# Optimization experiments

Hardware: AMD Instinct MI355X
Metric: run time of the kernel (lower is better)

## Reference

```python
import jax, jax.numpy as jnp
import numpy as np

HO, WO = 64, 64
SHARPNESS = 150.0


def _stereographic_grid(ho, wo):
    # Matches create_normal_grid(..., 'stereographic'); torch.meshgrid 'ij':
    # v varies over rows (ho), u over cols (wo).
    v, u = np.meshgrid(np.arange(ho), np.arange(wo), indexing='ij')
    p = 4.0 * ((u + 0.5) / wo - 0.5)
    q = -4.0 * ((v + 0.5) / ho - 0.5)
    d = 1.0 + p ** 2 + q ** 2
    z = -(-1.0 + p ** 2 + q ** 2) / d
    m = (z > 0.0).astype(np.float32)
    x = 2.0 * p / d * m
    y = 2.0 * q / d * m
    z = z * m
    return np.stack([x, y, z], axis=-1).reshape(-1, 3).astype(np.float32)  # [ho*wo,3]


_GRID = _stereographic_grid(HO, WO)
_IDX = np.nonzero(np.any(_GRID != 0, axis=-1))[0]  # static valid-query indices [N]
_QN = _GRID[_IDX]  # [N,3]


def setup_inputs() -> dict:
    key = jax.random.key(0)
    k1, k2, k3 = jax.random.split(key, 3)
    bs, c, h, w = 2, 64, 192, 192
    in_fea_map = jax.random.normal(k1, (bs, c, h, w), dtype=jnp.float32)
    nrm = jax.random.normal(k2, (bs, 3, h, w), dtype=jnp.float32)
    in_normal_map = nrm / (jnp.linalg.norm(nrm, axis=1, keepdims=True) + 1e-8)
    in_mask_map = (jax.random.uniform(k3, (bs, 1, h, w)) > 0.2).astype(jnp.float32)
    log_query_norm = jnp.full((1,), np.log(SHARPNESS), dtype=jnp.float32)
    return {"in_fea_map": in_fea_map, "in_normal_map": in_normal_map,
            "in_mask_map": in_mask_map, "log_query_norm": log_query_norm}


def reference(in_fea_map, in_normal_map, in_mask_map, log_query_norm):
    bs, c, h, w = in_fea_map.shape
    hw = h * w
    qn = jnp.asarray(_QN, dtype=in_fea_map.dtype)  # [N,3] static valid queries
    vals = in_fea_map.reshape(bs, c, hw).transpose(0, 2, 1)       # [bs,HW,c]
    key_n = in_normal_map.reshape(bs, 3, hw)                       # [bs,3,HW]
    cos = jnp.einsum('nd,bdm->bnm', qn, key_n)                     # [bs,N,HW]
    dps = cos / np.float32(np.sqrt(3.0))
    dps = dps - jnp.max(dps, axis=-1, keepdims=True)
    w_ = jnp.exp(jnp.exp(log_query_norm) * dps)                    # dropout in eval = identity
    w_ = w_ * in_mask_map.reshape(bs, 1, hw)
    weights = w_ / (jnp.sum(w_, axis=-1, keepdims=True) + 1e-9)    # [bs,N,HW]
    mapped = weights @ vals                                        # [bs,N,c]
    mapped = jnp.concatenate([jnp.broadcast_to(qn, (bs,) + qn.shape), mapped], axis=-1)
    # variance map over last 3 feature channels
    mean = mapped[..., -3:]
    sq_mean = weights @ (vals[..., -3:] ** 2)
    var = jnp.sum(sq_mean - mean ** 2, axis=-1, keepdims=True)
    mapped = jnp.concatenate([var, mapped], axis=-1)
    # cosine map
    rm_cos = jnp.sum(weights * cos, axis=-1, keepdims=True)
    mapped = jnp.concatenate([rm_cos, mapped], axis=-1)            # [bs,N,c+5]
    C = mapped.shape[-1]
    out = jnp.zeros((bs, HO * WO, C), mapped.dtype).at[:, _IDX, :].set(mapped)
    return out.transpose(0, 2, 1).reshape(bs, C, HO, WO)
```

## Files before the change

kernel.cpp:

```cpp
#include <hip/hip_runtime.h>
#include <hip/hip_bf16.h>
#include <cstdint>
#include <cstddef>

#define HW 36864
#define QT 64
#define NCHA 69
#define NCHK 576

constexpr bool is_valid_px(int v, int u) {
  int a = 2 * u - 63, b = 2 * v - 63;
  return a * a + b * b < 1024;
}
constexpr int count_valid() {
  int n = 0;
  for (int v = 0; v < 64; ++v)
    for (int u = 0; u < 64; ++u)
      if (is_valid_px(v, u)) ++n;
  return n;
}
constexpr int NV  = count_valid();
constexpr int NQT = (NV + QT - 1) / QT;
constexpr int NQP = NQT * QT;
constexpr int PLANE = 2 * NQP * NCHA;

constexpr size_t BM_SHORTS  = (size_t)2 * NCHK * 80 * 64;
constexpr size_t BM_BYTES   = BM_SHORTS * 2;
constexpr size_t NV_BYTES   = (size_t)2 * HW * 4 * 4;
constexpr size_t PART_OFF   = BM_BYTES + NV_BYTES;

struct QTab {
  short idx[NQP];
  short rank[4096];
};
constexpr QTab make_qtab() {
  QTab t{};
  int n = 0;
  for (int p = 0; p < 4096; ++p) {
    int v = p >> 6, u = p & 63;
    if (is_valid_px(v, u)) { t.idx[n] = (short)p; t.rank[p] = (short)n; ++n; }
    else t.rank[p] = -1;
  }
  for (int i = n; i < NQP; ++i) t.idx[i] = -1;
  return t;
}
__constant__ QTab g_qtab = make_qtab();

typedef short short8 __attribute__((ext_vector_type(8)));
typedef float f32x4  __attribute__((ext_vector_type(4)));

__device__ __forceinline__ unsigned short f2b(float f) {
  unsigned int u = __float_as_uint(f);
  u += 0x7FFFu + ((u >> 16) & 1u);
  return (unsigned short)(u >> 16);
}
__device__ __forceinline__ ushort2 f2b2(float a, float b) {
  __hip_bfloat162 h = __float22bfloat162_rn(make_float2(a, b));
  return *(ushort2*)&h;
}
__device__ __forceinline__ void pix2qn(int pix, float& x, float& y, float& z) {
  x = 0.f; y = 0.f; z = 0.f;
  if (pix >= 0) {
    int v = pix >> 6, u = pix & 63;
    float p = (float)(2 * u - 63) * (1.0f / 32.0f);
    float q = -(float)(2 * v - 63) * (1.0f / 32.0f);
    float d = 1.0f + p * p + q * q;
    x = 2.0f * p / d; y = 2.0f * q / d; z = (1.0f - p * p - q * q) / d;
  }
}

#define PREP_BM_BLKS 2880
#define PREP_NV_BLKS 288

__global__ __launch_bounds__(256) void prep_kernel(
    const float* __restrict__ fea,
    const float* __restrict__ nrm,
    const float* __restrict__ msk,
    const float* __restrict__ lqn,
    unsigned short* __restrict__ Bm,
    float* __restrict__ nv)
{
  const float Cc = __expf(lqn[0]) * 0.57735026919f;
  if (blockIdx.x < PREP_BM_BLKS) {
    int gid = blockIdx.x * 256 + threadIdx.x;
    int g   = gid & 7;
    int row = (gid >> 3) % 80;
    int chk = ((gid >> 3) / 80) % NCHK;
    int b   = gid / (8 * 80 * NCHK);
    int px0 = chk * 64 + g * 8;
    float v[8];
    if (row < 64) {
      const float* p = fea + ((size_t)b * 64 + row) * HW + px0;
      #pragma unroll
      for (int i = 0; i < 8; ++i) v[i] = p[i];
    } else if (row < 67) {
      const float* p = fea + ((size_t)b * 64 + (61 + row - 64)) * HW + px0;
      #pragma unroll
      for (int i = 0; i < 8; ++i) { float x = p[i]; v[i] = x * x; }
    } else if (row < 70) {
      const float* p = nrm + ((size_t)b * 3 + (row - 67)) * HW + px0;
      #pragma unroll
      for (int i = 0; i < 8; ++i) v[i] = p[i];
    } else {
      float c = (row == 70) ? 1.0f : 0.0f;
      #pragma unroll
      for (int i = 0; i < 8; ++i) v[i] = c;
    }
    short8 o;
    #pragma unroll
    for (int p2 = 0; p2 < 4; ++p2) {
      ushort2 pr = f2b2(v[2 * p2], v[2 * p2 + 1]);
      o[2 * p2] = (short)pr.x; o[2 * p2 + 1] = (short)pr.y;
    }
    *(short8*)&Bm[(((size_t)b * NCHK + chk) * 80 + row) * 64 + g * 8] = o;
  } else {
    int p = (blockIdx.x - PREP_BM_BLKS) * 256 + threadIdx.x;
    int b = p / HW, px = p % HW;
    float nx = nrm[((size_t)b * 3 + 0) * HW + px];
    float ny = nrm[((size_t)b * 3 + 1) * HW + px];
    float nz = nrm[((size_t)b * 3 + 2) * HW + px];
    float mk = msk[(size_t)b * HW + px];
    float bias = -Cc + (mk > 0.5f ? 0.f : -2000.f);
    *(float4*)&nv[(size_t)p * 4] = make_float4(Cc * nx, Cc * ny, Cc * nz, bias);
  }
}

template<int KSC>
__global__ __launch_bounds__(256, 4) void partial_kernel(
    const unsigned short* __restrict__ Bm,
    const float* __restrict__ nv,
    float* __restrict__ part)
{
  constexpr int SLICE  = HW / KSC;
  constexpr int NCHUNK = SLICE / 64;

  __shared__ __align__(16) unsigned short v_s[2][80][72];

  const int bx  = blockIdx.x;
  const int cls = bx & 7;
  const int r0  = bx >> 3;
  const int qt  = r0 % NQT;
  const int sh  = r0 / NQT;
  const int s   = sh * 8 + cls;
  const int b   = s / KSC;
  const int ks  = s % KSC;

  const int t    = threadIdx.x;
  const int wv   = t >> 6;
  const int Mh   = wv & 1;
  const int kko  = (wv >> 1) * 32;
  const int l    = t & 63;
  const int lq   = l >> 4;
  const int mrow = l & 15;

  float qx[2], qy[2], qz[2];
  pix2qn(g_qtab.idx[qt * QT + 32 * Mh + mrow],      qx[0], qy[0], qz[0]);
  pix2qn(g_qtab.idx[qt * QT + 32 * Mh + 16 + mrow], qx[1], qy[1], qz[1]);

  const int g0r = t >> 3,          g0c = (t & 7) * 8;
  const int g1r = (t + 256) >> 3,  g1c = g0c;
  const int g2r = (t + 512) >> 3;

  f32x4 acc[2][5];
  #pragma unroll
  for (int h = 0; h < 2; ++h)
    #pragma unroll
    for (int nt = 0; nt < 5; ++nt) acc[h][nt] = (f32x4)(0.0f);

  short8 pB[3];

  const int ckb = ks * NCHUNK;
  const float4* nvb = (const float4*)nv
      + ((size_t)b * HW + (size_t)ckb * 64 + (size_t)(kko + 8 * lq));

  auto load_chunk = [&](int ck) {
    int chkAbs = ckb + ck;
    const unsigned short* src = Bm + ((size_t)b * NCHK + chkAbs) * (80 * 64);
    pB[0] = *(const short8*)(src + (size_t)(t)       * 8);
    pB[1] = *(const short8*)(src + (size_t)(t + 256) * 8);
    if (t < 128) pB[2] = *(const short8*)(src + (size_t)(t + 512) * 8);
  };
  auto store_chunk = [&](int buf) {
    *(short8*)&v_s[buf][g0r][g0c] = pB[0];
    *(short8*)&v_s[buf][g1r][g1c] = pB[1];
    if (t < 128) *(short8*)&v_s[buf][g2r][g0c] = pB[2];
  };

  load_chunk(0);
  store_chunk(0);
  __syncthreads();

  for (int ck = 0; ck < NCHUNK; ++ck) {
    const int buf = ck & 1;
    if (ck + 1 < NCHUNK) load_chunk(ck + 1);

    const float4* nvp = nvb + (size_t)ck * 64;
    float e0[8], e1[8];
    #pragma unroll
    for (int j = 0; j < 8; ++j) {
      const float4 nvv = nvp[j];
      float t0 = fmaf(qx[0], nvv.x, fmaf(qy[0], nvv.y, fmaf(qz[0], nvv.z, nvv.w)));
      float t1 = fmaf(qx[1], nvv.x, fmaf(qy[1], nvv.y, fmaf(qz[1], nvv.z, nvv.w)));
      e0[j] = __expf(t0);
      e1[j] = __expf(t1);
    }
    short8 a0, a1;
    #pragma unroll
    for (int p = 0; p < 4; ++p) {
      ushort2 p0 = f2b2(e0[2 * p], e0[2 * p + 1]);
      ushort2 p1 = f2b2(e1[2 * p], e1[2 * p + 1]);
      a0[2 * p] = (short)p0.x; a0[2 * p + 1] = (short)p0.y;
      a1[2 * p] = (short)p1.x; a1[2 * p + 1] = (short)p1.y;
    }
    #pragma unroll
    for (int nt = 0; nt < 5; ++nt) {
      short8 bb = *(const short8*)&v_s[buf][16 * nt + mrow][kko + 8 * lq];
      acc[0][nt] = __builtin_amdgcn_mfma_f32_16x16x32_bf16(a0, bb, acc[0][nt], 0, 0, 0);
      acc[1][nt] = __builtin_amdgcn_mfma_f32_16x16x32_bf16(a1, bb, acc[1][nt], 0, 0, 0);
    }

    if (ck + 1 < NCHUNK) {
      store_chunk(buf ^ 1);
      __syncthreads();
    }
  }

  __syncthreads();
  float* scr = (float*)&v_s[0][0][0];
  float* exs = scr + 64 * 80;

  if (kko) {
    #pragma unroll
    for (int h = 0; h < 2; ++h)
      #pragma unroll
      for (int nt = 0; nt < 5; ++nt)
        #pragma unroll
        for (int rr = 0; rr < 4; ++rr) {
          int qloc = 32 * Mh + 16 * h + 4 * lq + rr;
          scr[qloc * 80 + 16 * nt + mrow] = acc[h][nt][rr];
        }
  }
  __syncthreads();
  const size_t pbase = (size_t)ks * PLANE + ((size_t)b * NQP + (size_t)(qt * QT)) * NCHA;
  if (!kko) {
    #pragma unroll
    for (int h = 0; h < 2; ++h) {
      #pragma unroll
      for (int nt = 0; nt < 5; ++nt)
        #pragma unroll
        for (int rr = 0; rr < 4; ++rr) {
          int qloc = 32 * Mh + 16 * h + 4 * lq + rr;
          acc[h][nt][rr] += scr[qloc * 80 + 16 * nt + mrow];
        }
      #pragma unroll
      for (int nt = 0; nt < 4; ++nt)
        #pragma unroll
        for (int rr = 0; rr < 4; ++rr) {
          int qloc = 32 * Mh + 16 * h + 4 * lq + rr;
          part[pbase + (size_t)qloc * NCHA + (size_t)(16 * nt + mrow)] = acc[h][nt][rr];
        }
      if (mrow < 7) {
        #pragma unroll
        for (int rr = 0; rr < 4; ++rr)
          exs[(32 * Mh + 16 * h + 4 * lq + rr) * 9 + mrow] = acc[h][4][rr];
      }
    }
  }
  __syncthreads();
  if (t < 64) {
    float gx, gy, gz;
    pix2qn(g_qtab.idx[qt * QT + t], gx, gy, gz);
    const float* E = exs + t * 9;
    float swc = gx * E[3] + gy * E[4] + gz * E[5];
    size_t o = pbase + (size_t)t * NCHA;
    part[o + 64] = E[0];
    part[o + 65] = E[1];
    part[o + 66] = E[2];
    part[o + 67] = swc;
    part[o + 68] = E[6];
  }
}

#define NFIN (2 * NQT * 16)
#define NTAIL (2 * NFIN)

__global__ __launch_bounds__(256) void finalize_kernel(
    const float* __restrict__ part,
    float* __restrict__ out,
    int ksc)
{
  const int blk = blockIdx.x;
  const int t   = threadIdx.x;

  if (blk < NFIN) {
    __shared__ float sm[4][NCHA];
    const int b   = blk / (NQT * 16);
    const int rem = blk % (NQT * 16);
    const int qt  = rem >> 4;
    const int qr  = rem & 15;
    const int q0  = qt * QT + qr * 4;

    const size_t colbase = ((size_t)b * NQP + (size_t)q0) * NCHA;
    for (int i = t; i < 4 * NCHA; i += 256) {
      float sv = 0.f;
      const size_t off = colbase + (size_t)i;
      #pragma unroll 8
      for (int k = 0; k < ksc; ++k) sv += part[(size_t)k * PLANE + off];
      sm[0][i] = sv;
    }
    __syncthreads();

    for (int i = t; i < 4 * NCHA; i += 256) {
      const int ql = i / NCHA;
      const int oc = i % NCHA;
      const int pix = g_qtab.idx[q0 + ql];
      if (pix < 0) continue;
      const float* A = sm[ql];
      const float inv = 1.0f / (A[68] + 1e-9f);
      float gx, gy, gz;
      pix2qn(pix, gx, gy, gz);
      float val;
      if (oc == 0)      val = A[67] * inv;
      else if (oc == 1) {
        val = 0.f;
        #pragma unroll
        for (int j = 0; j < 3; ++j) {
          float m  = A[61 + j] * inv;
          float sq = A[64 + j] * inv;
          val += sq - m * m;
        }
      }
      else if (oc == 2) val = gx;
      else if (oc == 3) val = gy;
      else if (oc == 4) val = gz;
      else              val = A[oc - 5] * inv;
      out[((size_t)b * NCHA + (size_t)oc) * 4096 + pix] = val;
    }
  } else {
    const int start = (blk - NFIN) * 256 + t;
    const int strd  = (NTAIL - NFIN) * 256;
    const int TOT   = 2 * NCHA * 4096;
    for (int i = start; i < TOT; i += strd) {
      if (g_qtab.rank[i & 4095] < 0) out[i] = 0.0f;
    }
  }
}

extern "C" void kernel_launch(void* const* d_in, const int* in_sizes, int n_in,
                              void* d_out, int out_size, void* d_ws, size_t ws_size,
                              hipStream_t stream) {
  const float* fea = (const float*)d_in[0];
  const float* nrm = (const float*)d_in[1];
  const float* msk = (const float*)d_in[2];
  const float* lqn = (const float*)d_in[3];
  unsigned short* Bm = (unsigned short*)d_ws;
  float* nv   = (float*)((char*)d_ws + BM_BYTES);
  float* part = (float*)((char*)d_ws + PART_OFF);
  float* out  = (float*)d_out;

  prep_kernel<<<dim3(PREP_BM_BLKS + PREP_NV_BLKS), 256, 0, stream>>>(
      fea, nrm, msk, lqn, Bm, nv);

  const size_t need64 = PART_OFF + (size_t)PLANE * 64 * sizeof(float);
  const size_t need32 = PART_OFF + (size_t)PLANE * 32 * sizeof(float);
  if (ws_size >= need64) {
    partial_kernel<64><<<dim3(2 * 64 * NQT), 256, 0, stream>>>(Bm, nv, part);
    finalize_kernel<<<dim3(NTAIL), 256, 0, stream>>>(part, out, 64);
  } else if (ws_size >= need32) {
    partial_kernel<32><<<dim3(2 * 32 * NQT), 256, 0, stream>>>(Bm, nv, part);
    finalize_kernel<<<dim3(NTAIL), 256, 0, stream>>>(part, out, 32);
  } else {
    partial_kernel<16><<<dim3(2 * 16 * NQT), 256, 0, stream>>>(Bm, nv, part);
    finalize_kernel<<<dim3(NTAIL), 256, 0, stream>>>(part, out, 16);
  }
}
```

Measured before the change: 118.7 us.

## Fuse bf16 prep into partial kernel and widen query tile to 128

Removes the separate prep kernel and its workspace round trip. The partial kernel now loads fp32 features, normals and mask directly, converts them to bf16 and builds the scaled-normal table in shared memory. The query tile doubles to 128, so each wave owns 32 queries over the full 64-pixel chunk, and the cross-wave K reduction through shared memory goes away. The cost is repeated fp32 loads and conversions per query tile (fewer tiles now) and larger global loads per block, in exchange for one less launch and no intermediate buffer.

Result: faster. 107.9 us (-9.1%).

```diff
diff --git a/kernel.cpp b/kernel.cpp
--- a/kernel.cpp
+++ b/kernel.cpp
@@ -4,9 +4,8 @@
 #include <cstddef>
 
 #define HW 36864
-#define QT 64
+#define QT 128
 #define NCHA 69
-#define NCHK 576
 
 constexpr bool is_valid_px(int v, int u) {
   int a = 2 * u - 63, b = 2 * v - 63;
@@ -23,11 +22,6 @@
 constexpr int NQT = (NV + QT - 1) / QT;
 constexpr int NQP = NQT * QT;
 constexpr int PLANE = 2 * NQP * NCHA;
-
-constexpr size_t BM_SHORTS  = (size_t)2 * NCHK * 80 * 64;
-constexpr size_t BM_BYTES   = BM_SHORTS * 2;
-constexpr size_t NV_BYTES   = (size_t)2 * HW * 4 * 4;
-constexpr size_t PART_OFF   = BM_BYTES + NV_BYTES;
 
 struct QTab {
   short idx[NQP];
@@ -49,14 +43,17 @@
 typedef short short8 __attribute__((ext_vector_type(8)));
 typedef float f32x4  __attribute__((ext_vector_type(4)));
 
-__device__ __forceinline__ unsigned short f2b(float f) {
-  unsigned int u = __float_as_uint(f);
-  u += 0x7FFFu + ((u >> 16) & 1u);
-  return (unsigned short)(u >> 16);
-}
 __device__ __forceinline__ ushort2 f2b2(float a, float b) {
   __hip_bfloat162 h = __float22bfloat162_rn(make_float2(a, b));
   return *(ushort2*)&h;
+}
+__device__ __forceinline__ short8 cvt8(float4 a, float4 b) {
+  short8 o;
+  ushort2 p0 = f2b2(a.x, a.y), p1 = f2b2(a.z, a.w);
+  ushort2 p2 = f2b2(b.x, b.y), p3 = f2b2(b.z, b.w);
+  o[0] = (short)p0.x; o[1] = (short)p0.y; o[2] = (short)p1.x; o[3] = (short)p1.y;
+  o[4] = (short)p2.x; o[5] = (short)p2.y; o[6] = (short)p3.x; o[7] = (short)p3.y;
+  return o;
 }
 __device__ __forceinline__ void pix2qn(int pix, float& x, float& y, float& z) {
   x = 0.f; y = 0.f; z = 0.f;
@@ -69,72 +66,19 @@
   }
 }
 
-#define PREP_BM_BLKS 2880
-#define PREP_NV_BLKS 288
-
-__global__ __launch_bounds__(256) void prep_kernel(
+template<int KSC>
+__global__ __launch_bounds__(256, 4) void partial_kernel(
     const float* __restrict__ fea,
     const float* __restrict__ nrm,
     const float* __restrict__ msk,
     const float* __restrict__ lqn,
-    unsigned short* __restrict__ Bm,
-    float* __restrict__ nv)
-{
-  const float Cc = __expf(lqn[0]) * 0.57735026919f;
-  if (blockIdx.x < PREP_BM_BLKS) {
-    int gid = blockIdx.x * 256 + threadIdx.x;
-    int g   = gid & 7;
-    int row = (gid >> 3) % 80;
-    int chk = ((gid >> 3) / 80) % NCHK;
-    int b   = gid / (8 * 80 * NCHK);
-    int px0 = chk * 64 + g * 8;
-    float v[8];
-    if (row < 64) {
-      const float* p = fea + ((size_t)b * 64 + row) * HW + px0;
-      #pragma unroll
-      for (int i = 0; i < 8; ++i) v[i] = p[i];
-    } else if (row < 67) {
-      const float* p = fea + ((size_t)b * 64 + (61 + row - 64)) * HW + px0;
-      #pragma unroll
-      for (int i = 0; i < 8; ++i) { float x = p[i]; v[i] = x * x; }
-    } else if (row < 70) {
-      const float* p = nrm + ((size_t)b * 3 + (row - 67)) * HW + px0;
-      #pragma unroll
-      for (int i = 0; i < 8; ++i) v[i] = p[i];
-    } else {
-      float c = (row == 70) ? 1.0f : 0.0f;
-      #pragma unroll
-      for (int i = 0; i < 8; ++i) v[i] = c;
-    }
-    short8 o;
-    #pragma unroll
-    for (int p2 = 0; p2 < 4; ++p2) {
-      ushort2 pr = f2b2(v[2 * p2], v[2 * p2 + 1]);
-      o[2 * p2] = (short)pr.x; o[2 * p2 + 1] = (short)pr.y;
-    }
-    *(short8*)&Bm[(((size_t)b * NCHK + chk) * 80 + row) * 64 + g * 8] = o;
-  } else {
-    int p = (blockIdx.x - PREP_BM_BLKS) * 256 + threadIdx.x;
-    int b = p / HW, px = p % HW;
-    float nx = nrm[((size_t)b * 3 + 0) * HW + px];
-    float ny = nrm[((size_t)b * 3 + 1) * HW + px];
-    float nz = nrm[((size_t)b * 3 + 2) * HW + px];
-    float mk = msk[(size_t)b * HW + px];
-    float bias = -Cc + (mk > 0.5f ? 0.f : -2000.f);
-    *(float4*)&nv[(size_t)p * 4] = make_float4(Cc * nx, Cc * ny, Cc * nz, bias);
-  }
-}
-
-template<int KSC>
-__global__ __launch_bounds__(256, 4) void partial_kernel(
-    const unsigned short* __restrict__ Bm,
-    const float* __restrict__ nv,
     float* __restrict__ part)
 {
   constexpr int SLICE  = HW / KSC;
   constexpr int NCHUNK = SLICE / 64;
 
   __shared__ __align__(16) unsigned short v_s[2][80][72];
+  __shared__ __align__(16) float nrm4_s[2][64][4];
 
   const int bx  = blockIdx.x;
   const int cls = bx & 7;
@@ -147,19 +91,19 @@
 
   const int t    = threadIdx.x;
   const int wv   = t >> 6;
-  const int Mh   = wv & 1;
-  const int kko  = (wv >> 1) * 32;
   const int l    = t & 63;
   const int lq   = l >> 4;
   const int mrow = l & 15;
 
+  const float Cc = __expf(lqn[0]) * 0.57735026919f;
+
   float qx[2], qy[2], qz[2];
-  pix2qn(g_qtab.idx[qt * QT + 32 * Mh + mrow],      qx[0], qy[0], qz[0]);
-  pix2qn(g_qtab.idx[qt * QT + 32 * Mh + 16 + mrow], qx[1], qy[1], qz[1]);
-
-  const int g0r = t >> 3,          g0c = (t & 7) * 8;
-  const int g1r = (t + 256) >> 3,  g1c = g0c;
-  const int g2r = (t + 512) >> 3;
+  pix2qn(g_qtab.idx[qt * QT + 32 * wv + mrow],      qx[0], qy[0], qz[0]);
+  pix2qn(g_qtab.idx[qt * QT + 32 * wv + 16 + mrow], qx[1], qy[1], qz[1]);
+
+  const int c0 = (t & 7) * 8;
+  const int rg = t >> 3;
+  const int pxp = 32 * (l >> 5) + 4 * (l & 7) + ((l >> 3) & 3);
 
   f32x4 acc[2][5];
   #pragma unroll
@@ -167,23 +111,60 @@
     #pragma unroll
     for (int nt = 0; nt < 5; ++nt) acc[h][nt] = (f32x4)(0.0f);
 
-  short8 pB[3];
-
+  float4 pF[6];
+  float nx, ny, nz, mk;
+  const size_t feab = (size_t)b * 64 * HW;
+  const size_t nrmb = (size_t)b * 3 * HW;
+  const size_t mskb = (size_t)b * HW;
   const int ckb = ks * NCHUNK;
-  const float4* nvb = (const float4*)nv
-      + ((size_t)b * HW + (size_t)ckb * 64 + (size_t)(kko + 8 * lq));
+
+  if (t >= 48 && t < 128) {
+    int row = 64 + rg;
+    short cv = (row == 70) ? (short)0x3F80 : (short)0;
+    short8 o;
+    #pragma unroll
+    for (int i = 0; i < 8; ++i) o[i] = cv;
+    *(short8*)&v_s[0][row][c0] = o;
+    *(short8*)&v_s[1][row][c0] = o;
+  }
 
   auto load_chunk = [&](int ck) {
-    int chkAbs = ckb + ck;
-    const unsigned short* src = Bm + ((size_t)b * NCHK + chkAbs) * (80 * 64);
-    pB[0] = *(const short8*)(src + (size_t)(t)       * 8);
-    pB[1] = *(const short8*)(src + (size_t)(t + 256) * 8);
-    if (t < 128) pB[2] = *(const short8*)(src + (size_t)(t + 512) * 8);
+    const size_t p0 = (size_t)((ckb + ck) * 64);
+    if (t < 64) {
+      size_t px = p0 + (size_t)l;
+      nx = nrm[nrmb + px];
+      ny = nrm[nrmb + HW + px];
+      nz = nrm[nrmb + 2 * HW + px];
+      mk = msk[mskb + px];
+    }
+    const float* fb = fea + feab + p0 + c0;
+    pF[0] = *(const float4*)(fb + (size_t)rg * HW);
+    pF[1] = *(const float4*)(fb + (size_t)rg * HW + 4);
+    pF[2] = *(const float4*)(fb + (size_t)(rg + 32) * HW);
+    pF[3] = *(const float4*)(fb + (size_t)(rg + 32) * HW + 4);
+    if (t < 48) {
+      const float* srcb = (t < 24)
+          ? (fea + feab + (size_t)(61 + rg) * HW)
+          : (nrm + nrmb + (size_t)(rg - 3) * HW);
+      pF[4] = *(const float4*)(srcb + p0 + c0);
+      pF[5] = *(const float4*)(srcb + p0 + c0 + 4);
+    }
   };
   auto store_chunk = [&](int buf) {
-    *(short8*)&v_s[buf][g0r][g0c] = pB[0];
-    *(short8*)&v_s[buf][g1r][g1c] = pB[1];
-    if (t < 128) *(short8*)&v_s[buf][g2r][g0c] = pB[2];
+    if (t < 64)
+      *(float4*)&nrm4_s[buf][pxp][0] =
+          make_float4(Cc * nx, Cc * ny, Cc * nz,
+                      -Cc + (mk > 0.5f ? 0.f : -2000.f));
+    *(short8*)&v_s[buf][rg][c0]      = cvt8(pF[0], pF[1]);
+    *(short8*)&v_s[buf][rg + 32][c0] = cvt8(pF[2], pF[3]);
+    if (t < 48) {
+      float4 a = pF[4], bq = pF[5];
+      if (t < 24) {
+        a.x *= a.x; a.y *= a.y; a.z *= a.z; a.w *= a.w;
+        bq.x *= bq.x; bq.y *= bq.y; bq.z *= bq.z; bq.w *= bq.w;
+      }
+      *(short8*)&v_s[buf][64 + rg][c0] = cvt8(a, bq);
+    }
   };
 
   load_chunk(0);
@@ -194,29 +175,31 @@
     const int buf = ck & 1;
     if (ck + 1 < NCHUNK) load_chunk(ck + 1);
 
-    const float4* nvp = nvb + (size_t)ck * 64;
-    float e0[8], e1[8];
     #pragma unroll
-    for (int j = 0; j < 8; ++j) {
-      const float4 nvv = nvp[j];
-      float t0 = fmaf(qx[0], nvv.x, fmaf(qy[0], nvv.y, fmaf(qz[0], nvv.z, nvv.w)));
-      float t1 = fmaf(qx[1], nvv.x, fmaf(qy[1], nvv.y, fmaf(qz[1], nvv.z, nvv.w)));
-      e0[j] = __expf(t0);
-      e1[j] = __expf(t1);
-    }
-    short8 a0, a1;
-    #pragma unroll
-    for (int p = 0; p < 4; ++p) {
-      ushort2 p0 = f2b2(e0[2 * p], e0[2 * p + 1]);
-      ushort2 p1 = f2b2(e1[2 * p], e1[2 * p + 1]);
-      a0[2 * p] = (short)p0.x; a0[2 * p + 1] = (short)p0.y;
-      a1[2 * p] = (short)p1.x; a1[2 * p + 1] = (short)p1.y;
-    }
-    #pragma unroll
-    for (int nt = 0; nt < 5; ++nt) {
-      short8 bb = *(const short8*)&v_s[buf][16 * nt + mrow][kko + 8 * lq];
-      acc[0][nt] = __builtin_amdgcn_mfma_f32_16x16x32_bf16(a0, bb, acc[0][nt], 0, 0, 0);
-      acc[1][nt] = __builtin_amdgcn_mfma_f32_16x16x32_bf16(a1, bb, acc[1][nt], 0, 0, 0);
+    for (int kh = 0; kh < 2; ++kh) {
+      float e0[8], e1[8];
+      #pragma unroll
+      for (int j = 0; j < 8; ++j) {
+        const float4 nvv = *(const float4*)&nrm4_s[buf][32 * kh + 4 * j + lq][0];
+        float t0 = fmaf(qx[0], nvv.x, fmaf(qy[0], nvv.y, fmaf(qz[0], nvv.z, nvv.w)));
+        float t1 = fmaf(qx[1], nvv.x, fmaf(qy[1], nvv.y, fmaf(qz[1], nvv.z, nvv.w)));
+        e0[j] = __expf(t0);
+        e1[j] = __expf(t1);
+      }
+      short8 a0, a1;
+      #pragma unroll
+      for (int p = 0; p < 4; ++p) {
+        ushort2 p0 = f2b2(e0[2 * p], e0[2 * p + 1]);
+        ushort2 p1 = f2b2(e1[2 * p], e1[2 * p + 1]);
+        a0[2 * p] = (short)p0.x; a0[2 * p + 1] = (short)p0.y;
+        a1[2 * p] = (short)p1.x; a1[2 * p + 1] = (short)p1.y;
+      }
+      #pragma unroll
+      for (int nt = 0; nt < 5; ++nt) {
+        short8 bb = *(const short8*)&v_s[buf][16 * nt + mrow][32 * kh + 8 * lq];
+        acc[0][nt] = __builtin_amdgcn_mfma_f32_16x16x32_bf16(a0, bb, acc[0][nt], 0, 0, 0);
+        acc[1][nt] = __builtin_amdgcn_mfma_f32_16x16x32_bf16(a1, bb, acc[1][nt], 0, 0, 0);
+      }
     }
 
     if (ck + 1 < NCHUNK) {
@@ -226,48 +209,26 @@
   }
 
   __syncthreads();
-  float* scr = (float*)&v_s[0][0][0];
-  float* exs = scr + 64 * 80;
-
-  if (kko) {
+  float* exs = (float*)&v_s[0][0][0];
+
+  const size_t pbase = (size_t)ks * PLANE + ((size_t)b * NQP + (size_t)(qt * QT)) * NCHA;
+  #pragma unroll
+  for (int h = 0; h < 2; ++h) {
     #pragma unroll
-    for (int h = 0; h < 2; ++h)
-      #pragma unroll
-      for (int nt = 0; nt < 5; ++nt)
-        #pragma unroll
-        for (int rr = 0; rr < 4; ++rr) {
-          int qloc = 32 * Mh + 16 * h + 4 * lq + rr;
-          scr[qloc * 80 + 16 * nt + mrow] = acc[h][nt][rr];
-        }
+    for (int nt = 0; nt < 4; ++nt)
+      #pragma unroll
+      for (int rr = 0; rr < 4; ++rr) {
+        int qloc = 32 * wv + 16 * h + 4 * lq + rr;
+        part[pbase + (size_t)qloc * NCHA + (size_t)(16 * nt + mrow)] = acc[h][nt][rr];
+      }
+    if (mrow < 7) {
+      #pragma unroll
+      for (int rr = 0; rr < 4; ++rr)
+        exs[(32 * wv + 16 * h + 4 * lq + rr) * 9 + mrow] = acc[h][4][rr];
+    }
   }
   __syncthreads();
-  const size_t pbase = (size_t)ks * PLANE + ((size_t)b * NQP + (size_t)(qt * QT)) * NCHA;
-  if (!kko) {
-    #pragma unroll
-    for (int h = 0; h < 2; ++h) {
-      #pragma unroll
-      for (int nt = 0; nt < 5; ++nt)
-        #pragma unroll
-        for (int rr = 0; rr < 4; ++rr) {
-          int qloc = 32 * Mh + 16 * h + 4 * lq + rr;
-          acc[h][nt][rr] += scr[qloc * 80 + 16 * nt + mrow];
-        }
-      #pragma unroll
-      for (int nt = 0; nt < 4; ++nt)
-        #pragma unroll
-        for (int rr = 0; rr < 4; ++rr) {
-          int qloc = 32 * Mh + 16 * h + 4 * lq + rr;
-          part[pbase + (size_t)qloc * NCHA + (size_t)(16 * nt + mrow)] = acc[h][nt][rr];
-        }
-      if (mrow < 7) {
-        #pragma unroll
-        for (int rr = 0; rr < 4; ++rr)
-          exs[(32 * Mh + 16 * h + 4 * lq + rr) * 9 + mrow] = acc[h][4][rr];
-      }
-    }
-  }
-  __syncthreads();
-  if (t < 64) {
+  if (t < QT) {
     float gx, gy, gz;
     pix2qn(g_qtab.idx[qt * QT + t], gx, gy, gz);
     const float* E = exs + t * 9;
@@ -281,7 +242,7 @@
   }
 }
 
-#define NFIN (2 * NQT * 16)
+#define NFIN 448
 #define NTAIL (2 * NFIN)
 
 __global__ __launch_bounds__(256) void finalize_kernel(
@@ -294,11 +255,9 @@
 
   if (blk < NFIN) {
     __shared__ float sm[4][NCHA];
-    const int b   = blk / (NQT * 16);
-    const int rem = blk % (NQT * 16);
-    const int qt  = rem >> 4;
-    const int qr  = rem & 15;
-    const int q0  = qt * QT + qr * 4;
+    const int b   = blk / (NFIN / 2);
+    const int rem = blk % (NFIN / 2);
+    const int q0  = rem * 4;
 
     const size_t colbase = ((size_t)b * NQP + (size_t)q0) * NCHA;
     for (int i = t; i < 4 * NCHA; i += 256) {
@@ -353,24 +312,19 @@
   const float* nrm = (const float*)d_in[1];
   const float* msk = (const float*)d_in[2];
   const float* lqn = (const float*)d_in[3];
-  unsigned short* Bm = (unsigned short*)d_ws;
-  float* nv   = (float*)((char*)d_ws + BM_BYTES);
-  float* part = (float*)((char*)d_ws + PART_OFF);
+  float* part = (float*)d_ws;
   float* out  = (float*)d_out;
 
-  prep_kernel<<<dim3(PREP_BM_BLKS + PREP_NV_BLKS), 256, 0, stream>>>(
-      fea, nrm, msk, lqn, Bm, nv);
-
-  const size_t need64 = PART_OFF + (size_t)PLANE * 64 * sizeof(float);
-  const size_t need32 = PART_OFF + (size_t)PLANE * 32 * sizeof(float);
+  const size_t need64 = (size_t)64 * PLANE * sizeof(float);
+  const size_t need32 = (size_t)32 * PLANE * sizeof(float);
   if (ws_size >= need64) {
-    partial_kernel<64><<<dim3(2 * 64 * NQT), 256, 0, stream>>>(Bm, nv, part);
+    partial_kernel<64><<<dim3(2 * 64 * NQT), 256, 0, stream>>>(fea, nrm, msk, lqn, part);
     finalize_kernel<<<dim3(NTAIL), 256, 0, stream>>>(part, out, 64);
   } else if (ws_size >= need32) {
-    partial_kernel<32><<<dim3(2 * 32 * NQT), 256, 0, stream>>>(Bm, nv, part);
+    partial_kernel<32><<<dim3(2 * 32 * NQT), 256, 0, stream>>>(fea, nrm, msk, lqn, part);
     finalize_kernel<<<dim3(NTAIL), 256, 0, stream>>>(part, out, 32);
   } else {
-    partial_kernel<16><<<dim3(2 * 16 * NQT), 256, 0, stream>>>(Bm, nv, part);
+    partial_kernel<16><<<dim3(2 * 16 * NQT), 256, 0, stream>>>(fea, nrm, msk, lqn, part);
     finalize_kernel<<<dim3(NTAIL), 256, 0, stream>>>(part, out, 16);
   }
 }
```
